# Kernel optimization log

Hardware: AMD Instinct MI355X
Metric: run time of the kernel (lower is better)

Reference implementation:

```python
import jax, jax.numpy as jnp
import numpy as np

VTH = 1.0      # v_threshold
TAU = 2.0      # spikingjelly LIFNode default tau
ALPHA = 2.0    # ATan surrogate alpha
EPS = 1e-5     # BatchNorm eps
N_HEADS = 8
TOPK = 4       # routed regions per query region
REGION = 64    # tokens per region (4096 tokens -> 64 regions)


@jax.custom_vjp
def spike_fn(v):
    return (v >= VTH).astype(v.dtype)

def _spike_fwd(v):
    return (v >= VTH).astype(v.dtype), v

def _spike_bwd(v, g):
    sg = (ALPHA / 2.0) / (1.0 + (jnp.pi / 2.0 * ALPHA * (v - VTH)) ** 2)
    return (g * sg,)

spike_fn.defvjp(_spike_fwd, _spike_bwd)


def lif(x):
    # x: [T, B, L, D]; LIF with decay_input=True, hard reset to 0, detach_reset
    def step(v, xt):
        v = v + (xt - v) / TAU
        s = spike_fn(v)
        v = v * (1.0 - jax.lax.stop_gradient(s))
        return v, s
    _, s = jax.lax.scan(step, jnp.zeros_like(x[0]), x)
    return s


def batchnorm(x, gamma, beta):
    # torch BN1d over [T*B, D, L] in training mode == per-channel stats over (T,B,L)
    mean = x.mean(axis=(0, 1, 2))
    var = jnp.mean((x - mean) ** 2, axis=(0, 1, 2))
    return (x - mean) * jax.lax.rsqrt(var + EPS) * gamma + beta


def bilevel_attn(x, qkv_w, qkv_b, proj_w, proj_b):
    # x: [TB, L, D]
    TB, L, D = x.shape
    nreg = L // REGION
    hd = D // N_HEADS
    qkv = x @ qkv_w.T + qkv_b
    q, k, v = jnp.split(qkv, 3, axis=-1)
    qr = q.reshape(TB, nreg, REGION, D)
    kr = k.reshape(TB, nreg, REGION, D)
    vr = v.reshape(TB, nreg, REGION, D)
    # coarse region-level routing via mean-pooled q/k affinity
    aff = jnp.einsum('bnd,bmd->bnm', qr.mean(2), kr.mean(2))  # [TB, nreg, nreg]
    _, idx = jax.lax.top_k(aff, TOPK)                         # [TB, nreg, TOPK]
    gather = jax.vmap(lambda t, ix: t[ix])                    # per-sample region gather
    kg = gather(kr, idx).reshape(TB, nreg, TOPK * REGION, N_HEADS, hd)
    vg = gather(vr, idx).reshape(TB, nreg, TOPK * REGION, N_HEADS, hd)
    qh = qr.reshape(TB, nreg, REGION, N_HEADS, hd)
    logits = jnp.einsum('bnqhd,bnkhd->bnhqk', qh, kg) * (hd ** -0.5)
    p = jax.nn.softmax(logits, axis=-1)
    o = jnp.einsum('bnhqk,bnkhd->bnqhd', p, vg).reshape(TB, L, D)
    return o @ proj_w.T + proj_b


def setup_inputs() -> dict:
    key = jax.random.key(0)
    ks = jax.random.split(key, 8)
    T, B, Lt, L, D = 4, 2, 4, 1024, 256
    Ltot = Lt * L
    s = 0.02
    return {
        'x': jax.random.normal(ks[0], (T, B, Ltot, D), jnp.float32),
        'bn1_g': jnp.ones((D,), jnp.float32),
        'bn1_b': jnp.zeros((D,), jnp.float32),
        'bn2_g': jnp.ones((D,), jnp.float32),
        'bn2_b': jnp.zeros((D,), jnp.float32),
        'qkv_w': jax.random.normal(ks[1], (3 * D, D), jnp.float32) * s,
        'qkv_b': jnp.zeros((3 * D,), jnp.float32),
        'proj_w': jax.random.normal(ks[2], (D, D), jnp.float32) * s,
        'proj_b': jnp.zeros((D,), jnp.float32),
        'ffn_w1': jax.random.normal(ks[3], (4 * D, D), jnp.float32) * s,
        'ffn_b1': jnp.zeros((4 * D,), jnp.float32),
        'ffn_w2': jax.random.normal(ks[4], (D, 4 * D), jnp.float32) * s,
        'ffn_b2': jnp.zeros((D,), jnp.float32),
        'scale': jnp.ones((1,), jnp.float32) * 0.5,
        'Lt': Lt, 'b': B, 'L': L, 'dim': D,
    }


def reference(x, bn1_g, bn1_b, bn2_g, bn2_b, qkv_w, qkv_b, proj_w, proj_b,
              ffn_w1, ffn_b1, ffn_w2, ffn_b2, scale, Lt, b, L, dim):
    T = x.shape[0]
    Ltot = Lt * L
    # attention branch
    identity = x
    s1 = lif(batchnorm(x, bn1_g, bn1_b))
    a = bilevel_attn(s1.reshape(T * b, Ltot, dim), qkv_w, qkv_b, proj_w, proj_b)
    x = identity + a.reshape(T, b, Ltot, dim) * scale
    # ffn branch
    s2 = lif(batchnorm(x, bn2_g, bn2_b))
    h = jax.nn.gelu(s2 @ ffn_w1.T + ffn_b1, approximate=False) @ ffn_w2.T + ffn_b2
    return x + h * scale
```

## Files before the change

kernel.cpp:

```cpp
#include <hip/hip_runtime.h>
#include <hip/hip_bf16.h>
#include <math.h>

typedef __attribute__((ext_vector_type(8))) short short8;
typedef __attribute__((ext_vector_type(4))) float f32x4;

#define DIM 256
#define NROWS 32768
#define PERT 2097152
#define SAMP_TOK 4096

__device__ __forceinline__ float b2f(__hip_bfloat16 h){ return __bfloat162float(h); }
__device__ __forceinline__ __hip_bfloat16 f2b(float f){ return __float2bfloat16(f); }
__device__ __forceinline__ unsigned short f2bu(float f){
  __hip_bfloat16 h = __float2bfloat16(f);
  unsigned short u; __builtin_memcpy(&u, &h, 2); return u;
}

#define GLD_LDS16(gp, lp) __builtin_amdgcn_global_load_lds( \
    (const __attribute__((address_space(1))) unsigned int*)(gp), \
    (__attribute__((address_space(3))) unsigned int*)(lp), 16, 0, 0)

__device__ __forceinline__ float gelu_fast(float v){
  float z  = v * 0.70710678118654752f;
  float az = fabsf(z);
  float t  = __builtin_amdgcn_rcpf(fmaf(0.3275911f, az, 1.0f));
  float p  = fmaf(fmaf(fmaf(fmaf(1.061405429f, t, -1.453152027f), t,
                            1.421413741f), t, -0.284496736f), t, 0.254829592f);
  p *= t;
  float e  = __expf(-z * z);
  float y  = fmaf(-p, e, 1.0f);
  return fmaf(0.5f * fabsf(v), y, 0.5f * v);
}

__global__ void f2ball_k(const float* __restrict__ w_qkv, const float* __restrict__ w_proj,
                         const float* __restrict__ w_f1, const float* __restrict__ w_f2,
                         __hip_bfloat16* __restrict__ o_qkv, __hip_bfloat16* __restrict__ o_proj,
                         __hip_bfloat16* __restrict__ o_f1, __hip_bfloat16* __restrict__ o_f2){
  int i = blockIdx.x * 256 + threadIdx.x;
  if (i < 196608)          o_qkv[i]           = f2b(w_qkv[i]);
  else if (i < 262144)     o_proj[i - 196608] = f2b(w_proj[i - 196608]);
  else if (i < 524288)     o_f1[i - 262144]   = f2b(w_f1[i - 262144]);
  else                     o_f2[i - 524288]   = f2b(w_f2[i - 524288]);
}

__global__ void bn_stats_k(const float* __restrict__ x, float* __restrict__ sum, float* __restrict__ sumsq){
  __shared__ __align__(16) float rs[4][256];
  __shared__ __align__(16) float rq[4][256];
  int t = threadIdx.x;
  int g = t & 63, r = t >> 6;
  size_t base = ((size_t)blockIdx.x * 128 + r) * DIM + g * 4;
  float4 s = {0.f,0.f,0.f,0.f}, q = {0.f,0.f,0.f,0.f};
  for (int i = 0; i < 32; ++i){
    float4 v = *reinterpret_cast<const float4*>(x + base + (size_t)i * 4 * DIM);
    s.x += v.x; s.y += v.y; s.z += v.z; s.w += v.w;
    q.x += v.x*v.x; q.y += v.y*v.y; q.z += v.z*v.z; q.w += v.w*v.w;
  }
  *reinterpret_cast<float4*>(&rs[r][g*4]) = s;
  *reinterpret_cast<float4*>(&rq[r][g*4]) = q;
  __syncthreads();
  int c = t;
  atomicAdd(&sum[c],   rs[0][c] + rs[1][c] + rs[2][c] + rs[3][c]);
  atomicAdd(&sumsq[c], rq[0][c] + rq[1][c] + rq[2][c] + rq[3][c]);
}

__global__ void bn_fin_k(const float* __restrict__ sum, const float* __restrict__ sumsq,
                         const float* __restrict__ g, const float* __restrict__ b,
                         float* __restrict__ a_out, float* __restrict__ b_out){
  int c = threadIdx.x;
  float mean = sum[c] * (1.f/32768.f);
  float var  = sumsq[c] * (1.f/32768.f) - mean*mean;
  float a = g[c] / sqrtf(var + 1e-5f);
  a_out[c] = a;
  b_out[c] = b[c] - mean * a;
}

__global__ void bn_red_k(const float* __restrict__ pps, const float* __restrict__ ppq,
                         const float* __restrict__ g, const float* __restrict__ b,
                         float* __restrict__ a_out, float* __restrict__ b_out){
  int c = threadIdx.x;
  float s = 0.f, q = 0.f;
  for (int r = 0; r < 512; ++r){
    s += pps[r * 256 + c];
    q += ppq[r * 256 + c];
  }
  float mean = s * (1.f/32768.f);
  float var  = q * (1.f/32768.f) - mean*mean;
  float a = g[c] / sqrtf(var + 1e-5f);
  a_out[c] = a;
  b_out[c] = b[c] - mean * a;
}

__global__ void lif_k(const float* __restrict__ x, const float* __restrict__ av,
                      const float* __restrict__ bv, __hip_bfloat16* __restrict__ s){
  int i = blockIdx.x * 256 + threadIdx.x;
  int e4 = i * 4;
  int c4 = e4 & (DIM - 1);
  float4 a = *reinterpret_cast<const float4*>(av + c4);
  float4 b = *reinterpret_cast<const float4*>(bv + c4);
  float4 v = {0.f,0.f,0.f,0.f};
  #pragma unroll
  for (int t = 0; t < 4; ++t){
    float4 xn = *reinterpret_cast<const float4*>(x + (size_t)t * PERT + e4);
    xn.x = fmaf(xn.x, a.x, b.x); xn.y = fmaf(xn.y, a.y, b.y);
    xn.z = fmaf(xn.z, a.z, b.z); xn.w = fmaf(xn.w, a.w, b.w);
    v.x += (xn.x - v.x) * 0.5f; v.y += (xn.y - v.y) * 0.5f;
    v.z += (xn.z - v.z) * 0.5f; v.w += (xn.w - v.w) * 0.5f;
    ushort4 sp;
    sp.x = (v.x >= 1.0f) ? 0x3F80 : 0;  v.x = (v.x >= 1.0f) ? 0.f : v.x;
    sp.y = (v.y >= 1.0f) ? 0x3F80 : 0;  v.y = (v.y >= 1.0f) ? 0.f : v.y;
    sp.z = (v.z >= 1.0f) ? 0x3F80 : 0;  v.z = (v.z >= 1.0f) ? 0.f : v.z;
    sp.w = (v.w >= 1.0f) ? 0x3F80 : 0;  v.w = (v.w >= 1.0f) ? 0.f : v.w;
    *reinterpret_cast<ushort4*>(reinterpret_cast<unsigned short*>(s) + (size_t)t * PERT + e4) = sp;
  }
}

__global__ void region_sum_k(const __hip_bfloat16* __restrict__ s, float* __restrict__ sm){
  __shared__ __align__(16) float red[4][256];
  int r = blockIdx.x, t = threadIdx.x;
  int g = t & 63, sub = t >> 6;
  const unsigned short* sp = reinterpret_cast<const unsigned short*>(s);
  size_t base = ((size_t)r * 64 + sub * 16) * DIM + g * 4;
  float4 acc = {0.f,0.f,0.f,0.f};
  for (int i = 0; i < 16; ++i){
    ushort4 u = *reinterpret_cast<const ushort4*>(sp + base + (size_t)i * DIM);
    acc.x += (u.x != 0) ? 1.f : 0.f; acc.y += (u.y != 0) ? 1.f : 0.f;
    acc.z += (u.z != 0) ? 1.f : 0.f; acc.w += (u.w != 0) ? 1.f : 0.f;
  }
  *reinterpret_cast<float4*>(&red[sub][g*4]) = acc;
  __syncthreads();
  if (sub == 0){
    float4 o;
    o.x = (red[0][g*4+0] + red[1][g*4+0] + red[2][g*4+0] + red[3][g*4+0]) * 0.015625f;
    o.y = (red[0][g*4+1] + red[1][g*4+1] + red[2][g*4+1] + red[3][g*4+1]) * 0.015625f;
    o.z = (red[0][g*4+2] + red[1][g*4+2] + red[2][g*4+2] + red[3][g*4+2]) * 0.015625f;
    o.w = (red[0][g*4+3] + red[1][g*4+3] + red[2][g*4+3] + red[3][g*4+3]) * 0.015625f;
    *reinterpret_cast<float4*>(sm + (size_t)r * DIM + g * 4) = o;
  }
}

__global__ void rgemm_k(const float* __restrict__ smr, const float* __restrict__ w,
                        const float* __restrict__ bias, float* __restrict__ qkm){
  __shared__ float arow[256];
  int r = blockIdx.x, t = threadIdx.x;
  arow[t] = smr[(size_t)r * 256 + t];
  __syncthreads();
  for (int j = t; j < 512; j += 256){
    const float* wr = w + (size_t)j * 256;
    float acc = 0.f;
    for (int k = 0; k < 256; ++k) acc += arow[k] * wr[k];
    qkm[(size_t)r * 512 + j] = acc + bias[j];
  }
}

template<int EPI>
__global__ __launch_bounds__(256) void gemm_bt(
    const __hip_bfloat16* __restrict__ A, const __hip_bfloat16* __restrict__ W,
    const float* __restrict__ bias, void* __restrict__ outp,
    const void* __restrict__ extra, const float* __restrict__ scaleptr,
    float* __restrict__ pps, float* __restrict__ ppq,
    int K, int N)
{
  __shared__ __align__(16) short As0[128 * 32];
  __shared__ __align__(16) short Ws0[128 * 32];
  __shared__ __align__(16) short As1[128 * 32];
  __shared__ __align__(16) short Ws1[128 * 32];
  int tid = threadIdx.x;
  int bm = blockIdx.x, bn = blockIdx.y;
  int lane = tid & 63;
  int l16 = lane & 15, quad = lane >> 4;
  int wv = tid >> 6;
  int wm = (wv >> 1) << 6, wn = (wv & 1) << 6;

  const int srow = tid >> 2;
  const int sq   = (tid & 3) ^ ((srow >> 1) & 3);
  const __hip_bfloat16* Ag = A + (size_t)(bm * 128 + srow) * K + (sq << 3);
  const __hip_bfloat16* Wg = W + (size_t)(bn * 128 + srow) * K + (sq << 3);
  const size_t rstep = (size_t)64 * K;

  int roA[4], roW[4];
  #pragma unroll
  for (int i = 0; i < 4; ++i){
    int Ra = wm + i * 16 + l16;
    roA[i] = Ra * 32 + ((quad ^ ((Ra >> 1) & 3)) << 3);
    int Rw = wn + i * 16 + l16;
    roW[i] = Rw * 32 + ((quad ^ ((Rw >> 1) & 3)) << 3);
  }

  f32x4 zero = {0.f, 0.f, 0.f, 0.f};
  f32x4 acc[4][4];
  #pragma unroll
  for (int i = 0; i < 4; ++i)
    #pragma unroll
    for (int j = 0; j < 4; ++j) acc[i][j] = zero;

  auto stage = [&](short* Ad, short* Wd, int k0){
    GLD_LDS16(Ag + k0,         Ad + tid * 8);
    GLD_LDS16(Ag + rstep + k0, Ad + tid * 8 + 2048);
    GLD_LDS16(Wg + k0,         Wd + tid * 8);
    GLD_LDS16(Wg + rstep + k0, Wd + tid * 8 + 2048);
  };
  auto compute = [&](const short* Asb, const short* Wsb){
    short8 af[4];
    #pragma unroll
    for (int mi = 0; mi < 4; ++mi)
      af[mi] = *reinterpret_cast<const short8*>(Asb + roA[mi]);
    #pragma unroll
    for (int ni = 0; ni < 4; ++ni){
      short8 wf = *reinterpret_cast<const short8*>(Wsb + roW[ni]);
      #pragma unroll
      for (int mi = 0; mi < 4; ++mi)
        acc[mi][ni] = __builtin_amdgcn_mfma_f32_16x16x32_bf16(wf, af[mi], acc[mi][ni], 0, 0, 0);
    }
  };

  stage(As0, Ws0, 0);
  __syncthreads();
  for (int k0 = 0; k0 < K; k0 += 64){
    if (k0 + 32 < K) stage(As1, Ws1, k0 + 32);
    compute(As0, Ws0);
    __syncthreads();
    if (k0 + 64 < K) stage(As0, Ws0, k0 + 64);
    if (k0 + 32 < K) compute(As1, Ws1);
    __syncthreads();
  }

  if (EPI == 0){
    short* Cw = (wv == 0) ? As0 : (wv == 1) ? Ws0 : (wv == 2) ? As1 : Ws1;
    #pragma unroll
    for (int ni = 0; ni < 4; ++ni){
      int col0 = (bn << 7) + wn + ni * 16 + (quad << 2);
      float4 bv = *reinterpret_cast<const float4*>(bias + col0);
      #pragma unroll
      for (int mi = 0; mi < 4; ++mi){
        float v0 = acc[mi][ni][0] + bv.x;
        float v1 = acc[mi][ni][1] + bv.y;
        float v2 = acc[mi][ni][2] + bv.z;
        float v3 = acc[mi][ni][3] + bv.w;
        unsigned lo = (unsigned)f2bu(v0) | ((unsigned)f2bu(v1) << 16);
        unsigned hi = (unsigned)f2bu(v2) | ((unsigned)f2bu(v3) << 16);
        int row = mi * 16 + l16;
        int cb  = (ni * 32 + (quad << 3)) ^ ((row & 7) << 4);
        *reinterpret_cast<uint2*>(reinterpret_cast<char*>(Cw) + row * 128 + cb) =
            make_uint2(lo, hi);
      }
    }
    asm volatile("s_waitcnt lgkmcnt(0)" ::: "memory");
    #pragma unroll
    for (int p = 0; p < 8; ++p){
      int row = p * 8 + (lane >> 3);
      int cb  = ((lane & 7) << 4) ^ ((row & 7) << 4);
      uint4 val = *reinterpret_cast<const uint4*>(
          reinterpret_cast<const char*>(Cw) + row * 128 + cb);
      int rowg = (bm << 7) + wm + row;
      int colg = (bn << 7) + wn + ((lane & 7) << 3);
      *reinterpret_cast<uint4*>((__hip_bfloat16*)outp + (size_t)rowg * N + colg) = val;
    }
  } else {
    float sc = scaleptr[0];
    float4 ts[4], tq[4];
    #pragma unroll
    for (int ni = 0; ni < 4; ++ni){ ts[ni] = {0.f,0.f,0.f,0.f}; tq[ni] = {0.f,0.f,0.f,0.f}; }
    #pragma unroll
    for (int ni = 0; ni < 4; ++ni){
      int col0 = (bn << 7) + wn + ni * 16 + (quad << 2);
      float4 bv = *reinterpret_cast<const float4*>(bias + col0);
      #pragma unroll
      for (int mi = 0; mi < 4; ++mi){
        int rowg = (bm << 7) + wm + mi * 16 + l16;
        size_t off = (size_t)rowg * N + col0;
        float v0 = acc[mi][ni][0] + bv.x;
        float v1 = acc[mi][ni][1] + bv.y;
        float v2 = acc[mi][ni][2] + bv.z;
        float v3 = acc[mi][ni][3] + bv.w;
        float4 xr = *reinterpret_cast<const float4*>((const float*)extra + off);
        float4 ov;
        ov.x = xr.x + v0 * sc; ov.y = xr.y + v1 * sc;
        ov.z = xr.z + v2 * sc; ov.w = xr.w + v3 * sc;
        *reinterpret_cast<float4*>((float*)outp + off) = ov;
        ts[ni].x += ov.x; ts[ni].y += ov.y; ts[ni].z += ov.z; ts[ni].w += ov.w;
        tq[ni].x += ov.x*ov.x; tq[ni].y += ov.y*ov.y;
        tq[ni].z += ov.z*ov.z; tq[ni].w += ov.w*ov.w;
      }
    }
    int prow = (bm << 1) + (wm >> 6);
    #pragma unroll
    for (int ni = 0; ni < 4; ++ni){
      float4 S = ts[ni], Q = tq[ni];
      #pragma unroll
      for (int m = 1; m < 16; m <<= 1){
        S.x += __shfl_xor(S.x, m); S.y += __shfl_xor(S.y, m);
        S.z += __shfl_xor(S.z, m); S.w += __shfl_xor(S.w, m);
        Q.x += __shfl_xor(Q.x, m); Q.y += __shfl_xor(Q.y, m);
        Q.z += __shfl_xor(Q.z, m); Q.w += __shfl_xor(Q.w, m);
      }
      if (l16 == 0){
        int col0 = (bn << 7) + wn + ni * 16 + (quad << 2);
        *reinterpret_cast<float4*>(pps + prow * 256 + col0) = S;
        *reinterpret_cast<float4*>(ppq + prow * 256 + col0) = Q;
      }
    }
  }
}

__global__ __launch_bounds__(256) void ffn_fused_k(
    const __hip_bfloat16* __restrict__ A,
    const __hip_bfloat16* __restrict__ W1,
    const float* __restrict__ b1,
    const __hip_bfloat16* __restrict__ W2,
    const float* __restrict__ b2,
    float* __restrict__ x2,
    const float* __restrict__ scaleptr)
{
  __shared__ __align__(16) short lds[24832];
  const int tid = threadIdx.x;
  const int bm = blockIdx.x;
  const int lane = tid & 63;
  const int l16 = lane & 15, quad = lane >> 4;
  const int wv = tid >> 6;

  const int srow = tid >> 2;
  const int sq   = (tid & 3) ^ ((srow >> 1) & 3);
  const __hip_bfloat16* Ag = A + (size_t)(bm * 64 + srow) * 256 + (sq << 3);

  int roA[4], roH[4], roW1[2], roW2[4];
  #pragma unroll
  for (int mi = 0; mi < 4; ++mi){
    int Ra = mi * 16 + l16;
    roA[mi] = Ra * 32 + ((quad ^ ((Ra >> 1) & 3)) << 3);
    roH[mi] = 16384 + Ra * 132 + (quad << 3);
  }
  #pragma unroll
  for (int ni = 0; ni < 2; ++ni){
    int Rw = wv * 32 + ni * 16 + l16;
    roW1[ni] = Rw * 32 + ((quad ^ ((Rw >> 1) & 3)) << 3);
  }
  #pragma unroll
  for (int ni = 0; ni < 4; ++ni){
    int Rw = wv * 64 + ni * 16 + l16;
    roW2[ni] = Rw * 32 + ((quad ^ ((Rw >> 1) & 3)) << 3);
  }

  f32x4 zero = {0.f, 0.f, 0.f, 0.f};
  f32x4 acc2[4][4];
  #pragma unroll
  for (int i = 0; i < 4; ++i)
    #pragma unroll
    for (int j = 0; j < 4; ++j) acc2[i][j] = zero;

  for (int c1 = 0; c1 < 8; ++c1){
    f32x4 acc1[4][2];
    #pragma unroll
    for (int i = 0; i < 4; ++i){ acc1[i][0] = zero; acc1[i][1] = zero; }

    const __hip_bfloat16* W1g = W1 + (size_t)(c1 * 128 + srow) * 256 + (sq << 3);

    auto stage1 = [&](int off, int k0){
      GLD_LDS16(Ag + k0,              lds + off + tid * 8);
      GLD_LDS16(W1g + k0,             lds + off + 2048 + tid * 8);
      GLD_LDS16(W1g + 64 * 256 + k0,  lds + off + 2048 + tid * 8 + 2048);
    };
    stage1(0, 0);
    __syncthreads();
    #pragma unroll
    for (int k = 0; k < 8; ++k){
      const int cur = (k & 1) ? 6144 : 0;
      const int nxt = (k & 1) ? 0 : 6144;
      if (k < 7) stage1(nxt, (k + 1) * 32);
      short8 af[4];
      #pragma unroll
      for (int mi = 0; mi < 4; ++mi)
        af[mi] = *reinterpret_cast<const short8*>(lds + cur + roA[mi]);
      #pragma unroll
      for (int ni = 0; ni < 2; ++ni){
        short8 wf = *reinterpret_cast<const short8*>(lds + cur + 2048 + roW1[ni]);
        #pragma unroll
        for (int mi = 0; mi < 4; ++mi)
          acc1[mi][ni] = __builtin_amdgcn_mfma_f32_16x16x32_bf16(wf, af[mi], acc1[mi][ni], 0, 0, 0);
      }
      __syncthreads();
    }

    auto stageW2 = [&](int off, int kk){
      const __hip_bfloat16* p = W2 + (size_t)srow * 1024 + c1 * 128 + kk * 32 + (sq << 3);
      #pragma unroll
      for (int j = 0; j < 4; ++j)
        GLD_LDS16(p + (size_t)j * 64 * 1024, lds + off + tid * 8 + j * 2048);
    };
    stageW2(0, 0);
    #pragma unroll
    for (int ni = 0; ni < 2; ++ni){
      int colg = c1 * 128 + wv * 32 + ni * 16 + (quad << 2);
      float4 bv = *reinterpret_cast<const float4*>(b1 + colg);
      #pragma unroll
      for (int mi = 0; mi < 4; ++mi){
        float g0 = gelu_fast(acc1[mi][ni][0] + bv.x);
        float g1 = gelu_fast(acc1[mi][ni][1] + bv.y);
        float g2 = gelu_fast(acc1[mi][ni][2] + bv.z);
        float g3 = gelu_fast(acc1[mi][ni][3] + bv.w);
        unsigned lo = (unsigned)f2bu(g0) | ((unsigned)f2bu(g1) << 16);
        unsigned hi = (unsigned)f2bu(g2) | ((unsigned)f2bu(g3) << 16);
        *reinterpret_cast<uint2*>(
            lds + 16384 + (mi * 16 + l16) * 132 + wv * 32 + ni * 16 + (quad << 2)) =
            make_uint2(lo, hi);
      }
    }
    __syncthreads();

    #pragma unroll
    for (int kk = 0; kk < 4; ++kk){
      const int cur = (kk & 1) ? 8192 : 0;
      const int nxt = (kk & 1) ? 0 : 8192;
      if (kk < 3) stageW2(nxt, kk + 1);
      short8 af[4];
      #pragma unroll
      for (int mi = 0; mi < 4; ++mi)
        af[mi] = *reinterpret_cast<const short8*>(lds + roH[mi] + kk * 32);
      #pragma unroll
      for (int ni = 0; ni < 4; ++ni){
        short8 wf = *reinterpret_cast<const short8*>(lds + cur + roW2[ni]);
        #pragma unroll
        for (int mi = 0; mi < 4; ++mi)
          acc2[mi][ni] = __builtin_amdgcn_mfma_f32_16x16x32_bf16(wf, af[mi], acc2[mi][ni], 0, 0, 0);
      }
      __syncthreads();
    }
  }

  float sc = scaleptr[0];
  #pragma unroll
  for (int ni = 0; ni < 4; ++ni){
    int col0 = wv * 64 + ni * 16 + (quad << 2);
    float4 bv = *reinterpret_cast<const float4*>(b2 + col0);
    #pragma unroll
    for (int mi = 0; mi < 4; ++mi){
      int rowg = bm * 64 + mi * 16 + l16;
      size_t off = (size_t)rowg * 256 + col0;
      float4 xr = *reinterpret_cast<const float4*>(x2 + off);
      float4 ov;
      ov.x = xr.x + (acc2[mi][ni][0] + bv.x) * sc;
      ov.y = xr.y + (acc2[mi][ni][1] + bv.y) * sc;
      ov.z = xr.z + (acc2[mi][ni][2] + bv.z) * sc;
      ov.w = xr.w + (acc2[mi][ni][3] + bv.w) * sc;
      *reinterpret_cast<float4*>(x2 + off) = ov;
    }
  }
}

__global__ void topk_k(const float* __restrict__ qkm, int* __restrict__ idx){
  __shared__ float aff[64];
  int r = blockIdx.x;
  int m = threadIdx.x;
  int b = r >> 6;
  const float4* qrow = reinterpret_cast<const float4*>(qkm + (size_t)r * 512);
  const float4* krow = reinterpret_cast<const float4*>(qkm + (size_t)(b * 64 + m) * 512 + 256);
  float dot = 0.f;
  for (int d = 0; d < 64; ++d){
    float4 qv = qrow[d], kv = krow[d];
    dot += qv.x * kv.x + qv.y * kv.y + qv.z * kv.z + qv.w * kv.w;
  }
  aff[m] = dot;
  __syncthreads();
  if (m == 0){
    #pragma unroll
    for (int t = 0; t < 4; ++t){
      float best = -INFINITY; int bi = 0;
      for (int i = 0; i < 64; ++i){
        if (aff[i] > best){ best = aff[i]; bi = i; }
      }
      aff[bi] = -INFINITY;
      idx[r * 4 + t] = bi;
    }
  }
}

__global__ __launch_bounds__(256) void attn_mfma_k(
    const __hip_bfloat16* __restrict__ qkv, const int* __restrict__ idx,
    __hip_bfloat16* __restrict__ o_out, int rbase)
{
  __shared__ __align__(16) short lds[27136];
  const int rl = blockIdx.x;
  const int h  = blockIdx.y;
  const int rg = rbase + rl;
  const int bl = rl >> 6;
  const int tid = threadIdx.x;
  const int w = tid >> 6, lane = tid & 63;
  const int l16 = lane & 15, quad = lane >> 4;
  short* Pw = lds + 10240 + w * 4224;

  const int reg = idx[rg * 4 + (tid >> 6)] & 63;
  const size_t srow = (size_t)bl * SAMP_TOK + (size_t)reg * 64 + (tid & 63);
  const __hip_bfloat16* kvsrc = qkv + srow * 768 + 256 + (size_t)h * 32;

  const size_t qrow = (size_t)rl * 64 + w * 16 + l16;
  short8 qf = *reinterpret_cast<const short8*>(qkv + qrow * 768 + (size_t)h * 32 + quad * 8);

  uint4 vreg[4];
  #pragma unroll
  for (int c = 0; c < 4; ++c)
    vreg[c] = *reinterpret_cast<const uint4*>(kvsrc + 256 + c * 8);

  #pragma unroll
  for (int c = 0; c < 4; ++c)
    *reinterpret_cast<uint4*>(&lds[tid * 40 + c * 8]) =
      *reinterpret_cast<const uint4*>(kvsrc + c * 8);
  __syncthreads();

  f32x4 s[16];
  #pragma unroll
  for (int nt = 0; nt < 16; ++nt){
    short8 kf = *reinterpret_cast<const short8*>(&lds[(nt * 16 + l16) * 40 + quad * 8]);
    f32x4 z = {0.f, 0.f, 0.f, 0.f};
    s[nt] = __builtin_amdgcn_mfma_f32_16x16x32_bf16(kf, qf, z, 0, 0, 0);
  }
  __syncthreads();

  #pragma unroll
  for (int c = 0; c < 4; ++c){
    short8 vv = *reinterpret_cast<short8*>(&vreg[c]);
    #pragma unroll
    for (int e = 0; e < 8; ++e)
      lds[(c * 8 + e) * 264 + tid] = vv[e];
  }

  float mx = -1e30f;
  #pragma unroll
  for (int nt = 0; nt < 16; ++nt)
    #pragma unroll
    for (int r = 0; r < 4; ++r) mx = fmaxf(mx, s[nt][r]);
  mx = fmaxf(mx, __shfl_xor(mx, 16));
  mx = fmaxf(mx, __shfl_xor(mx, 32));
  float den = 0.f;
  #pragma unroll
  for (int nt = 0; nt < 16; ++nt)
    #pragma unroll
    for (int r = 0; r < 4; ++r){
      float e = __expf((s[nt][r] - mx) * 0.17677669529663687f);
      s[nt][r] = e; den += e;
    }
  den += __shfl_xor(den, 16);
  den += __shfl_xor(den, 32);

  #pragma unroll
  for (int nt = 0; nt < 16; ++nt){
    unsigned lo = (unsigned)f2bu(s[nt][0]) | ((unsigned)f2bu(s[nt][1]) << 16);
    unsigned hi = (unsigned)f2bu(s[nt][2]) | ((unsigned)f2bu(s[nt][3]) << 16);
    *reinterpret_cast<uint2*>(&Pw[l16 * 264 + nt * 16 + quad * 4]) = make_uint2(lo, hi);
  }
  __syncthreads();

  f32x4 o0 = {0.f, 0.f, 0.f, 0.f}, o1 = o0;
  #pragma unroll
  for (int kk = 0; kk < 8; ++kk){
    short8 pb = *reinterpret_cast<const short8*>(&Pw[l16 * 264 + kk * 32 + quad * 8]);
    short8 a0 = *reinterpret_cast<const short8*>(&lds[l16 * 264 + kk * 32 + quad * 8]);
    short8 a1 = *reinterpret_cast<const short8*>(&lds[(16 + l16) * 264 + kk * 32 + quad * 8]);
    o0 = __builtin_amdgcn_mfma_f32_16x16x32_bf16(a0, pb, o0, 0, 0, 0);
    o1 = __builtin_amdgcn_mfma_f32_16x16x32_bf16(a1, pb, o1, 0, 0, 0);
  }
  float inv = 1.f / den;
  size_t obase = ((size_t)rl * 64 + w * 16 + l16) * 256 + (size_t)h * 32;
  unsigned pk0 = (unsigned)f2bu(o0[0] * inv) | ((unsigned)f2bu(o0[1] * inv) << 16);
  unsigned pk1 = (unsigned)f2bu(o0[2] * inv) | ((unsigned)f2bu(o0[3] * inv) << 16);
  unsigned pk2 = (unsigned)f2bu(o1[0] * inv) | ((unsigned)f2bu(o1[1] * inv) << 16);
  unsigned pk3 = (unsigned)f2bu(o1[2] * inv) | ((unsigned)f2bu(o1[3] * inv) << 16);
  *reinterpret_cast<uint2*>(o_out + obase + quad * 4)      = make_uint2(pk0, pk1);
  *reinterpret_cast<uint2*>(o_out + obase + 16 + quad * 4) = make_uint2(pk2, pk3);
}

extern "C" void kernel_launch(void* const* d_in, const int* in_sizes, int n_in,
                              void* d_out, int out_size, void* d_ws, size_t ws_size,
                              hipStream_t stream)
{
  const float* x      = (const float*)d_in[0];
  const float* bn1_g  = (const float*)d_in[1];
  const float* bn1_b  = (const float*)d_in[2];
  const float* bn2_g  = (const float*)d_in[3];
  const float* bn2_b  = (const float*)d_in[4];
  const float* qkv_w  = (const float*)d_in[5];
  const float* qkv_b  = (const float*)d_in[6];
  const float* proj_w = (const float*)d_in[7];
  const float* proj_b = (const float*)d_in[8];
  const float* ffn_w1 = (const float*)d_in[9];
  const float* ffn_b1 = (const float*)d_in[10];
  const float* ffn_w2 = (const float*)d_in[11];
  const float* ffn_b2 = (const float*)d_in[12];
  const float* scale  = (const float*)d_in[13];
  float* x2 = (float*)d_out;

  char* ws = (char*)d_ws;
  const size_t MB = 1024 * 1024;
  float* sum1 = (float*)(ws + 0);
  float* sq1  = (float*)(ws + 1024);
  float* a1   = (float*)(ws + 4096);
  float* b1   = (float*)(ws + 5120);
  float* a2   = (float*)(ws + 6144);
  float* b2   = (float*)(ws + 7168);
  int*   idxb = (int*)(ws + 8192);
  float* smr  = (float*)(ws + 16384);
  float* qkm  = (float*)(ws + 540672);
  __hip_bfloat16* qkv_wb  = (__hip_bfloat16*)(ws + 1589248);
  __hip_bfloat16* proj_wb = (__hip_bfloat16*)(ws + 1982464);
  __hip_bfloat16* ffn_w1b = (__hip_bfloat16*)(ws + 2113536);
  __hip_bfloat16* ffn_w2b = (__hip_bfloat16*)(ws + 2637824);
  float* ppsum = (float*)(ws + 3162112);
  float* ppsq  = (float*)(ws + 3686400);
  __hip_bfloat16* s1 = (__hip_bfloat16*)(ws + 4 * MB);
  __hip_bfloat16* s2 = s1;
  char* chunkbuf = ws + 20 * MB;

  size_t avail = (ws_size > 20 * MB) ? (ws_size - 20 * MB) : (8 * MB);
  int nc = (avail >= 64 * MB) ? 8 : (avail >= 32 * MB) ? 4 : (avail >= 16 * MB) ? 2 : 1;

  __hip_bfloat16* qkvc = (__hip_bfloat16*)chunkbuf;
  __hip_bfloat16* oc   = (__hip_bfloat16*)(chunkbuf + (size_t)nc * 6 * MB);

  hipMemsetAsync(d_ws, 0, 4096, stream);

  f2ball_k<<<3072, 256, 0, stream>>>(qkv_w, proj_w, ffn_w1, ffn_w2,
                                     qkv_wb, proj_wb, ffn_w1b, ffn_w2b);

  bn_stats_k<<<256, 256, 0, stream>>>(x, sum1, sq1);
  bn_fin_k<<<1, 256, 0, stream>>>(sum1, sq1, bn1_g, bn1_b, a1, b1);
  lif_k<<<PERT / 1024, 256, 0, stream>>>(x, a1, b1, s1);
  region_sum_k<<<512, 256, 0, stream>>>(s1, smr);
  rgemm_k<<<512, 256, 0, stream>>>(smr, qkv_w, qkv_b, qkm);
  topk_k<<<512, 64, 0, stream>>>(qkm, idxb);

  const int nchunkA = 8 / nc;
  for (int c = 0; c < nchunkA; ++c){
    const size_t ro = (size_t)c * nc * SAMP_TOK;
    gemm_bt<0><<<dim3(nc * SAMP_TOK / 128, 6), 256, 0, stream>>>(
        s1 + ro * 256, qkv_wb, qkv_b, qkvc, nullptr, nullptr, nullptr, nullptr, 256, 768);
    attn_mfma_k<<<dim3(nc * 64, 8), 256, 0, stream>>>(qkvc, idxb, oc, c * nc * 64);
    gemm_bt<1><<<dim3(nc * SAMP_TOK / 128, 2), 256, 0, stream>>>(
        oc, proj_wb, proj_b, x2 + ro * 256, x + ro * 256, scale,
        ppsum + (ro >> 6) * 256, ppsq + (ro >> 6) * 256, 256, 256);
  }

  bn_red_k<<<1, 256, 0, stream>>>(ppsum, ppsq, bn2_g, bn2_b, a2, b2);
  lif_k<<<PERT / 1024, 256, 0, stream>>>(x2, a2, b2, s2);
  ffn_fused_k<<<512, 256, 0, stream>>>(s2, ffn_w1b, ffn_b1, ffn_w2b, ffn_b2, x2, scale);
}
```

Measured before the change: 357.5 us.

## Triple-buffer FFN GEMM1 loads with explicit vmcnt waits and swizzle hidden tile

The first FFN GEMM stage goes from double-buffered LDS staging with full __syncthreads to a three-deep ring buffer. Each iteration waits with s_waitcnt vmcnt(3) so one prefetch stays in flight across the barrier, hiding more global-load latency. The hidden-activation LDS tile also drops its padded stride of 132 for an XOR-swizzled stride of 128 to avoid bank conflicts. The change uses more LDS and depends on hand-written waitcnt counts being correct for the three loads issued per stage.

```diff
diff --git a/kernel.cpp b/kernel.cpp
--- a/kernel.cpp
+++ b/kernel.cpp
@@ -20,6 +20,10 @@
 #define GLD_LDS16(gp, lp) __builtin_amdgcn_global_load_lds( \
     (const __attribute__((address_space(1))) unsigned int*)(gp), \
     (__attribute__((address_space(3))) unsigned int*)(lp), 16, 0, 0)
+
+#define VMCNT3 asm volatile("s_waitcnt vmcnt(3)" ::: "memory")
+#define VMCNT0 asm volatile("s_waitcnt vmcnt(0)" ::: "memory")
+#define SBAR()  do { __builtin_amdgcn_s_barrier(); asm volatile("" ::: "memory"); } while(0)
 
 __device__ __forceinline__ float gelu_fast(float v){
   float z  = v * 0.70710678118654752f;
@@ -312,7 +316,7 @@
     float* __restrict__ x2,
     const float* __restrict__ scaleptr)
 {
-  __shared__ __align__(16) short lds[24832];
+  __shared__ __align__(16) short lds[26624];
   const int tid = threadIdx.x;
   const int bm = blockIdx.x;
   const int lane = tid & 63;
@@ -323,17 +327,18 @@
   const int sq   = (tid & 3) ^ ((srow >> 1) & 3);
   const __hip_bfloat16* Ag = A + (size_t)(bm * 64 + srow) * 256 + (sq << 3);
 
-  int roA[4], roH[4], roW1[2], roW2[4];
+  int roA[4], hbase[4], hx[4], roW1[2], roW2[4];
   #pragma unroll
   for (int mi = 0; mi < 4; ++mi){
     int Ra = mi * 16 + l16;
-    roA[mi] = Ra * 32 + ((quad ^ ((Ra >> 1) & 3)) << 3);
-    roH[mi] = 16384 + Ra * 132 + (quad << 3);
+    roA[mi]   = Ra * 32 + ((quad ^ ((Ra >> 1) & 3)) << 3);
+    hbase[mi] = 18432 + Ra * 128;
+    hx[mi]    = (Ra & 7) << 3;
   }
   #pragma unroll
   for (int ni = 0; ni < 2; ++ni){
     int Rw = wv * 32 + ni * 16 + l16;
-    roW1[ni] = Rw * 32 + ((quad ^ ((Rw >> 1) & 3)) << 3);
+    roW1[ni] = 2048 + Rw * 32 + ((quad ^ ((Rw >> 1) & 3)) << 3);
   }
   #pragma unroll
   for (int ni = 0; ni < 4; ++ni){
@@ -358,28 +363,30 @@
     auto stage1 = [&](int off, int k0){
       GLD_LDS16(Ag + k0,              lds + off + tid * 8);
       GLD_LDS16(W1g + k0,             lds + off + 2048 + tid * 8);
-      GLD_LDS16(W1g + 64 * 256 + k0,  lds + off + 2048 + tid * 8 + 2048);
+      GLD_LDS16(W1g + 64 * 256 + k0,  lds + off + 4096 + tid * 8);
     };
+
     stage1(0, 0);
-    __syncthreads();
+    stage1(6144, 32);
     #pragma unroll
     for (int k = 0; k < 8; ++k){
-      const int cur = (k & 1) ? 6144 : 0;
-      const int nxt = (k & 1) ? 0 : 6144;
-      if (k < 7) stage1(nxt, (k + 1) * 32);
+      if (k < 7) { VMCNT3; } else { VMCNT0; }
+      SBAR();
+      const int cur = (k % 3) * 6144;
+      if (k < 6) stage1(((k + 2) % 3) * 6144, (k + 2) * 32);
       short8 af[4];
       #pragma unroll
       for (int mi = 0; mi < 4; ++mi)
         af[mi] = *reinterpret_cast<const short8*>(lds + cur + roA[mi]);
       #pragma unroll
       for (int ni = 0; ni < 2; ++ni){
-        short8 wf = *reinterpret_cast<const short8*>(lds + cur + 2048 + roW1[ni]);
+        short8 wf = *reinterpret_cast<const short8*>(lds + cur + roW1[ni]);
         #pragma unroll
         for (int mi = 0; mi < 4; ++mi)
           acc1[mi][ni] = __builtin_amdgcn_mfma_f32_16x16x32_bf16(wf, af[mi], acc1[mi][ni], 0, 0, 0);
       }
-      __syncthreads();
-    }
+    }
+    SBAR();
 
     auto stageW2 = [&](int off, int kk){
       const __hip_bfloat16* p = W2 + (size_t)srow * 1024 + c1 * 128 + kk * 32 + (sq << 3);
@@ -388,6 +395,7 @@
         GLD_LDS16(p + (size_t)j * 64 * 1024, lds + off + tid * 8 + j * 2048);
     };
     stageW2(0, 0);
+
     #pragma unroll
     for (int ni = 0; ni < 2; ++ni){
       int colg = c1 * 128 + wv * 32 + ni * 16 + (quad << 2);
@@ -400,9 +408,9 @@
         float g3 = gelu_fast(acc1[mi][ni][3] + bv.w);
         unsigned lo = (unsigned)f2bu(g0) | ((unsigned)f2bu(g1) << 16);
         unsigned hi = (unsigned)f2bu(g2) | ((unsigned)f2bu(g3) << 16);
-        *reinterpret_cast<uint2*>(
-            lds + 16384 + (mi * 16 + l16) * 132 + wv * 32 + ni * 16 + (quad << 2)) =
-            make_uint2(lo, hi);
+        int row = mi * 16 + l16;
+        int hc  = (wv * 32 + ni * 16 + (quad << 2)) ^ ((row & 7) << 3);
+        *reinterpret_cast<uint2*>(lds + 18432 + row * 128 + hc) = make_uint2(lo, hi);
       }
     }
     __syncthreads();
@@ -414,8 +422,10 @@
       if (kk < 3) stageW2(nxt, kk + 1);
       short8 af[4];
       #pragma unroll
-      for (int mi = 0; mi < 4; ++mi)
-        af[mi] = *reinterpret_cast<const short8*>(lds + roH[mi] + kk * 32);
+      for (int mi = 0; mi < 4; ++mi){
+        int ha = hbase[mi] + (((kk << 5) + (quad << 3)) ^ hx[mi]);
+        af[mi] = *reinterpret_cast<const short8*>(lds + ha);
+      }
       #pragma unroll
       for (int ni = 0; ni < 4; ++ni){
         short8 wf = *reinterpret_cast<const short8*>(lds + cur + roW2[ni]);
```

New measurement: 349.8 us. 2.1% less time.

## Restructure fused FFN kernel to 512 threads with wider K stages

Applied to the files above, without the earlier changes.

The fused FFN kernel now runs with 8 waves per block instead of 4, so each wave owns half as many output columns in both GEMMs and holds fewer accumulators. The first GEMM now stages 64-wide K slices (four steps instead of eight) with a new XOR swizzle, and the GELU intermediate tile uses a swizzled 128-wide layout instead of padding. The aim is to cut register pressure, hide more latency with more waves, and halve the barrier count in the first GEMM. The cost is a larger LDS footprint (64 KB per block), which may limit blocks per CU, and more waves synchronising at each barrier.

```diff
diff --git a/kernel.cpp b/kernel.cpp
--- a/kernel.cpp
+++ b/kernel.cpp
@@ -303,7 +303,7 @@
   }
 }
 
-__global__ __launch_bounds__(256) void ffn_fused_k(
+__global__ __launch_bounds__(512, 4) void ffn_fused_k(
     const __hip_bfloat16* __restrict__ A,
     const __hip_bfloat16* __restrict__ W1,
     const float* __restrict__ b1,
@@ -312,112 +312,129 @@
     float* __restrict__ x2,
     const float* __restrict__ scaleptr)
 {
-  __shared__ __align__(16) short lds[24832];
+  __shared__ __align__(16) short lds[32768];
   const int tid = threadIdx.x;
   const int bm = blockIdx.x;
   const int lane = tid & 63;
   const int l16 = lane & 15, quad = lane >> 4;
   const int wv = tid >> 6;
 
-  const int srow = tid >> 2;
-  const int sq   = (tid & 3) ^ ((srow >> 1) & 3);
-  const __hip_bfloat16* Ag = A + (size_t)(bm * 64 + srow) * 256 + (sq << 3);
-
-  int roA[4], roH[4], roW1[2], roW2[4];
+  const int H = 0, S0 = 8192, S1 = 20480;
+
+  const int ar = tid >> 3, as = tid & 7;
+  const int asq = (as ^ (ar & 7)) << 3;
+  const __hip_bfloat16* Ag = A + (size_t)(bm * 64 + ar) * 256 + asq;
+  const int w2r = tid >> 2, w2s = tid & 3;
+  const int w2q = (w2s ^ (w2r & 3)) << 3;
+
+  int roA[4][2];
   #pragma unroll
   for (int mi = 0; mi < 4; ++mi){
     int Ra = mi * 16 + l16;
-    roA[mi] = Ra * 32 + ((quad ^ ((Ra >> 1) & 3)) << 3);
-    roH[mi] = 16384 + Ra * 132 + (quad << 3);
-  }
+    #pragma unroll
+    for (int kh = 0; kh < 2; ++kh)
+      roA[mi][kh] = Ra * 64 + ((((kh << 5) | (quad << 3)) ^ ((Ra & 7) << 3)));
+  }
+  int roW1[2];
+  {
+    int Rw = wv * 16 + l16;
+    #pragma unroll
+    for (int kh = 0; kh < 2; ++kh)
+      roW1[kh] = 4096 + Rw * 64 + ((((kh << 5) | (quad << 3)) ^ ((Rw & 7) << 3)));
+  }
+  int hwr[4], hrb[4];
+  const int hxor = l16 << 3;
+  #pragma unroll
+  for (int mi = 0; mi < 4; ++mi){
+    int row = mi * 16 + l16;
+    hwr[mi] = row * 128 + (((wv * 16 + quad * 4)) ^ hxor);
+    hrb[mi] = row * 128;
+  }
+  int roW2[2];
   #pragma unroll
   for (int ni = 0; ni < 2; ++ni){
     int Rw = wv * 32 + ni * 16 + l16;
-    roW1[ni] = Rw * 32 + ((quad ^ ((Rw >> 1) & 3)) << 3);
-  }
-  #pragma unroll
-  for (int ni = 0; ni < 4; ++ni){
-    int Rw = wv * 64 + ni * 16 + l16;
-    roW2[ni] = Rw * 32 + ((quad ^ ((Rw >> 1) & 3)) << 3);
+    roW2[ni] = Rw * 32 + (((quad ^ (Rw & 3))) << 3);
   }
 
   f32x4 zero = {0.f, 0.f, 0.f, 0.f};
-  f32x4 acc2[4][4];
-  #pragma unroll
-  for (int i = 0; i < 4; ++i)
-    #pragma unroll
-    for (int j = 0; j < 4; ++j) acc2[i][j] = zero;
+  f32x4 acc2[4][2];
+  #pragma unroll
+  for (int i = 0; i < 4; ++i){ acc2[i][0] = zero; acc2[i][1] = zero; }
+
+  float sc = scaleptr[0];
 
   for (int c1 = 0; c1 < 8; ++c1){
-    f32x4 acc1[4][2];
-    #pragma unroll
-    for (int i = 0; i < 4; ++i){ acc1[i][0] = zero; acc1[i][1] = zero; }
-
-    const __hip_bfloat16* W1g = W1 + (size_t)(c1 * 128 + srow) * 256 + (sq << 3);
-
-    auto stage1 = [&](int off, int k0){
-      GLD_LDS16(Ag + k0,              lds + off + tid * 8);
-      GLD_LDS16(W1g + k0,             lds + off + 2048 + tid * 8);
-      GLD_LDS16(W1g + 64 * 256 + k0,  lds + off + 2048 + tid * 8 + 2048);
+    f32x4 acc1[4];
+    #pragma unroll
+    for (int i = 0; i < 4; ++i) acc1[i] = zero;
+
+    const __hip_bfloat16* W1g = W1 + (size_t)(c1 * 128 + ar) * 256 + asq;
+
+    auto stage1 = [&](int S, int k0){
+      GLD_LDS16(Ag + k0,              lds + S + tid * 8);
+      GLD_LDS16(W1g + k0,             lds + S + 4096 + tid * 8);
+      GLD_LDS16(W1g + 64 * 256 + k0,  lds + S + 8192 + tid * 8);
     };
-    stage1(0, 0);
+    auto compute1 = [&](int S){
+      #pragma unroll
+      for (int kh = 0; kh < 2; ++kh){
+        short8 wf = *reinterpret_cast<const short8*>(lds + S + roW1[kh]);
+        #pragma unroll
+        for (int mi = 0; mi < 4; ++mi){
+          short8 af = *reinterpret_cast<const short8*>(lds + S + roA[mi][kh]);
+          acc1[mi] = __builtin_amdgcn_mfma_f32_16x16x32_bf16(wf, af, acc1[mi], 0, 0, 0);
+        }
+      }
+    };
+
+    stage1(S0, 0);
     __syncthreads();
     #pragma unroll
-    for (int k = 0; k < 8; ++k){
-      const int cur = (k & 1) ? 6144 : 0;
-      const int nxt = (k & 1) ? 0 : 6144;
-      if (k < 7) stage1(nxt, (k + 1) * 32);
-      short8 af[4];
-      #pragma unroll
-      for (int mi = 0; mi < 4; ++mi)
-        af[mi] = *reinterpret_cast<const short8*>(lds + cur + roA[mi]);
-      #pragma unroll
-      for (int ni = 0; ni < 2; ++ni){
-        short8 wf = *reinterpret_cast<const short8*>(lds + cur + 2048 + roW1[ni]);
-        #pragma unroll
-        for (int mi = 0; mi < 4; ++mi)
-          acc1[mi][ni] = __builtin_amdgcn_mfma_f32_16x16x32_bf16(wf, af[mi], acc1[mi][ni], 0, 0, 0);
-      }
+    for (int k = 0; k < 4; ++k){
+      const int cur = (k & 1) ? S1 : S0;
+      const int nxt = (k & 1) ? S0 : S1;
+      if (k < 3) stage1(nxt, (k + 1) * 64);
+      compute1(cur);
       __syncthreads();
     }
 
-    auto stageW2 = [&](int off, int kk){
-      const __hip_bfloat16* p = W2 + (size_t)srow * 1024 + c1 * 128 + kk * 32 + (sq << 3);
-      #pragma unroll
-      for (int j = 0; j < 4; ++j)
-        GLD_LDS16(p + (size_t)j * 64 * 1024, lds + off + tid * 8 + j * 2048);
+    auto stageW2 = [&](int S, int kk){
+      const __hip_bfloat16* p = W2 + (size_t)w2r * 1024 + c1 * 128 + kk * 32 + w2q;
+      GLD_LDS16(p,               lds + S + tid * 8);
+      GLD_LDS16(p + 128 * 1024,  lds + S + 4096 + tid * 8);
     };
-    stageW2(0, 0);
-    #pragma unroll
-    for (int ni = 0; ni < 2; ++ni){
-      int colg = c1 * 128 + wv * 32 + ni * 16 + (quad << 2);
+    stageW2(S0, 0);
+
+    {
+      int colg = c1 * 128 + wv * 16 + quad * 4;
       float4 bv = *reinterpret_cast<const float4*>(b1 + colg);
       #pragma unroll
       for (int mi = 0; mi < 4; ++mi){
-        float g0 = gelu_fast(acc1[mi][ni][0] + bv.x);
-        float g1 = gelu_fast(acc1[mi][ni][1] + bv.y);
-        float g2 = gelu_fast(acc1[mi][ni][2] + bv.z);
-        float g3 = gelu_fast(acc1[mi][ni][3] + bv.w);
+        float g0 = gelu_fast(acc1[mi][0] + bv.x);
+        float g1 = gelu_fast(acc1[mi][1] + bv.y);
+        float g2 = gelu_fast(acc1[mi][2] + bv.z);
+        float g3 = gelu_fast(acc1[mi][3] + bv.w);
         unsigned lo = (unsigned)f2bu(g0) | ((unsigned)f2bu(g1) << 16);
         unsigned hi = (unsigned)f2bu(g2) | ((unsigned)f2bu(g3) << 16);
-        *reinterpret_cast<uint2*>(
-            lds + 16384 + (mi * 16 + l16) * 132 + wv * 32 + ni * 16 + (quad << 2)) =
-            make_uint2(lo, hi);
+        *reinterpret_cast<uint2*>(lds + H + hwr[mi]) = make_uint2(lo, hi);
       }
     }
     __syncthreads();
 
     #pragma unroll
     for (int kk = 0; kk < 4; ++kk){
-      const int cur = (kk & 1) ? 8192 : 0;
-      const int nxt = (kk & 1) ? 0 : 8192;
+      const int cur = (kk & 1) ? S1 : S0;
+      const int nxt = (kk & 1) ? S0 : S1;
       if (kk < 3) stageW2(nxt, kk + 1);
       short8 af[4];
       #pragma unroll
-      for (int mi = 0; mi < 4; ++mi)
-        af[mi] = *reinterpret_cast<const short8*>(lds + roH[mi] + kk * 32);
-      #pragma unroll
-      for (int ni = 0; ni < 4; ++ni){
+      for (int mi = 0; mi < 4; ++mi){
+        int hc = (((kk << 5) | (quad << 3)) ^ hxor);
+        af[mi] = *reinterpret_cast<const short8*>(lds + H + hrb[mi] + hc);
+      }
+      #pragma unroll
+      for (int ni = 0; ni < 2; ++ni){
         short8 wf = *reinterpret_cast<const short8*>(lds + cur + roW2[ni]);
         #pragma unroll
         for (int mi = 0; mi < 4; ++mi)
@@ -427,10 +444,9 @@
     }
   }
 
-  float sc = scaleptr[0];
-  #pragma unroll
-  for (int ni = 0; ni < 4; ++ni){
-    int col0 = wv * 64 + ni * 16 + (quad << 2);
+  #pragma unroll
+  for (int ni = 0; ni < 2; ++ni){
+    int col0 = wv * 32 + ni * 16 + (quad << 2);
     float4 bv = *reinterpret_cast<const float4*>(b2 + col0);
     #pragma unroll
     for (int mi = 0; mi < 4; ++mi){
@@ -640,5 +656,5 @@
 
   bn_red_k<<<1, 256, 0, stream>>>(ppsum, ppsq, bn2_g, bn2_b, a2, b2);
   lif_k<<<PERT / 1024, 256, 0, stream>>>(x2, a2, b2, s2);
-  ffn_fused_k<<<512, 256, 0, stream>>>(s2, ffn_w1b, ffn_b1, ffn_w2b, ffn_b2, x2, scale);
-}
+  ffn_fused_k<<<512, 512, 0, stream>>>(s2, ffn_w1b, ffn_b1, ffn_w2b, ffn_b2, x2, scale);
+}
```

After: 347.9 us. -2.7%, faster.
